# Optimization experiments

Measured on AMD Instinct MI355X. Metric: run time of the kernel, lower is better.

The kernel has to match this reference:

```python
import jax, jax.numpy as jnp
import numpy as np

NUM_TOKENS = 8192
HIDDEN = 4096
NUM_EXPERTS = 64
TOP_K = 8


def setup_inputs() -> dict:
    key = jax.random.key(0)
    k1, k2, k3 = jax.random.split(key, 3)
    tokens = jax.random.normal(k1, (NUM_TOKENS, HIDDEN), dtype=jnp.float32)
    token_probs = jax.random.uniform(k2, (NUM_TOKENS, NUM_EXPERTS), dtype=jnp.float32)
    # exactly TOP_K experts per token -> static num_out_tokens
    scores = jax.random.normal(k3, (NUM_TOKENS, NUM_EXPERTS))
    _, topk_idx = jax.lax.top_k(scores, TOP_K)  # [T, K]
    rows = jnp.arange(NUM_TOKENS)[:, None]
    routing_map = jnp.zeros((NUM_TOKENS, NUM_EXPERTS), dtype=bool).at[rows, topk_idx].set(True)
    return {
        "tokens": tokens,
        "token_probs": token_probs,
        "routing_map": routing_map,
        "num_out_tokens": NUM_TOKENS * TOP_K,
    }


def reference(tokens, token_probs, routing_map, num_out_tokens):
    # Fallback (non-fused) path of TurboTokenPermuter.forward.
    num_tokens, _ = tokens.shape
    # routing_map.bool().T -> [E, T]; masked_select in row-major order =
    # for each expert (in order), the token ids routed to it (in token order).
    flat_mask = routing_map.T.reshape(-1)  # [E*T]
    # stable argsort of ~mask puts flat positions of True entries first, in order
    perm = jnp.argsort(~flat_mask, stable=True)[:num_out_tokens]  # flat E*T indices
    sorted_indices = (perm % num_tokens).astype(jnp.int32)  # token ids (column index)
    permuted_probs = token_probs.T.reshape(-1)[perm]
    permuted_input = tokens[sorted_indices]  # index_select along dim 0
    return permuted_input, permuted_probs, sorted_indices
```

## Files before the change

### kernel.cpp

```cpp
#include <hip/hip_runtime.h>
#include <stdint.h>

#define NTOK   8192
#define NEXP   64
#define HID    4096
#define OUTROW 65536
#define CHUNK  256
#define NCHUNK (NTOK / CHUNK)
#define NPART  (NEXP * NCHUNK)

typedef float f32x4 __attribute__((ext_vector_type(4)));

__global__ void pcount_kernel(const int* __restrict__ map, int* __restrict__ pcnt) {
    int b = blockIdx.x;
    int e = b >> 5, c = b & (NCHUNK - 1);
    int lane = threadIdx.x;
    int cnt = 0;
#pragma unroll
    for (int it = 0; it < CHUNK / 64; ++it) {
        int t = c * CHUNK + it * 64 + lane;
        bool m = map[(size_t)t * NEXP + e] != 0;
        cnt += __popcll(__ballot(m));
    }
    if (lane == 0) pcnt[b] = cnt;
}

__global__ void fused_kernel(const int* __restrict__ map,
                             const float* __restrict__ probs,
                             const int* __restrict__ pcnt,
                             const float* __restrict__ tokens,
                             float* __restrict__ out_rows,
                             float* __restrict__ out_probs,
                             float* __restrict__ out_idx) {
    int b = blockIdx.x;
    int e = b >> 5, c = b & (NCHUNK - 1);
    int tid = threadIdx.x;
    int w = tid >> 6, lane = tid & 63;

    __shared__ int red[256];
    __shared__ int wcnt[4];
    __shared__ int s_src[CHUNK];

    int acc = 0;
    for (int i = tid; i < b; i += 256) acc += pcnt[i];
    red[tid] = acc;
    __syncthreads();
    for (int off = 128; off > 0; off >>= 1) {
        if (tid < off) red[tid] += red[tid + off];
        __syncthreads();
    }
    int base = red[0];

    int t = c * CHUNK + w * 64 + lane;
    bool m = map[(size_t)t * NEXP + e] != 0;
    unsigned long long bal = __ballot(m);
    int rank = __popcll(bal & ((1ull << lane) - 1ull));
    if (lane == 0) wcnt[w] = __popcll(bal);
    __syncthreads();
    int wbase = 0;
#pragma unroll
    for (int i = 0; i < 4; ++i) wbase += (i < w) ? wcnt[i] : 0;
    int total = wcnt[0] + wcnt[1] + wcnt[2] + wcnt[3];

    if (m) {
        int local = wbase + rank;
        int pos = base + local;
        out_idx[pos] = (float)t;
        out_probs[pos] = probs[(size_t)t * NEXP + e];
        s_src[local] = t;
    }
    __syncthreads();

    for (int j = w; j < total; j += 4) {
        unsigned src = (unsigned)s_src[j];
        if (src >= NTOK) src = 0;
        const f32x4* sp = (const f32x4*)(tokens + (size_t)src * HID);
        f32x4* dp = (f32x4*)(out_rows + (size_t)(base + j) * HID);
#pragma unroll
        for (int k = 0; k < HID / 4 / 64; ++k) {
            f32x4 v = sp[lane + k * 64];
            __builtin_nontemporal_store(v, dp + lane + k * 64);
        }
    }
}

extern "C" void kernel_launch(void* const* d_in, const int* in_sizes, int n_in,
                              void* d_out, int out_size, void* d_ws, size_t ws_size,
                              hipStream_t stream) {
    const float* tokens = (const float*)d_in[0];
    const float* probs  = (const float*)d_in[1];
    const int*   map    = (const int*)d_in[2];

    float* out_rows  = (float*)d_out;
    float* out_probs = out_rows + (size_t)OUTROW * HID;
    float* out_idx   = out_probs + OUTROW;

    int* pcnt = (int*)d_ws;

    pcount_kernel<<<NPART, 64, 0, stream>>>(map, pcnt);
    fused_kernel<<<NPART, CHUNK, 0, stream>>>(map, probs, pcnt, tokens,
                                              out_rows, out_probs, out_idx);
}
```

Before: 295.2 us.

## Invert gather to per-token scatter, reading each token row once

The row copy moves out of the per-expert blocks into a separate gather kernel with one block per token. An assign kernel records each token's TOPK output positions in a workspace table using atomics, and the gather kernel loads the token row once and stores it to all of its destinations. This cuts source reads from one per output row to one per token and evens out the work per block. In exchange it adds a third launch, a workspace table that must be zeroed, and atomics, and it relies on every token having exactly TOPK experts.

```diff
diff --git a/kernel.cpp b/kernel.cpp
--- a/kernel.cpp
+++ b/kernel.cpp
@@ -4,6 +4,7 @@
 #define NTOK   8192
 #define NEXP   64
 #define HID    4096
+#define TOPK   8
 #define OUTROW 65536
 #define CHUNK  256
 #define NCHUNK (NTOK / CHUNK)
@@ -11,7 +12,8 @@
 
 typedef float f32x4 __attribute__((ext_vector_type(4)));
 
-__global__ void pcount_kernel(const int* __restrict__ map, int* __restrict__ pcnt) {
+__global__ void pcount_kernel(const int* __restrict__ map, int* __restrict__ pcnt,
+                              int* __restrict__ tok_cnt) {
     int b = blockIdx.x;
     int e = b >> 5, c = b & (NCHUNK - 1);
     int lane = threadIdx.x;
@@ -19,19 +21,19 @@
 #pragma unroll
     for (int it = 0; it < CHUNK / 64; ++it) {
         int t = c * CHUNK + it * 64 + lane;
-        bool m = map[(size_t)t * NEXP + e] != 0;
-        cnt += __popcll(__ballot(m));
+        cnt += __popcll(__ballot(map[(size_t)t * NEXP + e] != 0));
     }
     if (lane == 0) pcnt[b] = cnt;
+    if (lane < NTOK / NPART) tok_cnt[b * (NTOK / NPART) + lane] = 0;
 }
 
-__global__ void fused_kernel(const int* __restrict__ map,
-                             const float* __restrict__ probs,
-                             const int* __restrict__ pcnt,
-                             const float* __restrict__ tokens,
-                             float* __restrict__ out_rows,
-                             float* __restrict__ out_probs,
-                             float* __restrict__ out_idx) {
+__global__ void assign_kernel(const int* __restrict__ map,
+                              const float* __restrict__ probs,
+                              const int* __restrict__ pcnt,
+                              int* __restrict__ tok_cnt,
+                              int* __restrict__ tok_pos,
+                              float* __restrict__ probs_out,
+                              float* __restrict__ idx_out) {
     int b = blockIdx.x;
     int e = b >> 5, c = b & (NCHUNK - 1);
     int tid = threadIdx.x;
@@ -39,7 +41,6 @@
 
     __shared__ int red[256];
     __shared__ int wcnt[4];
-    __shared__ int s_src[CHUNK];
 
     int acc = 0;
     for (int i = tid; i < b; i += 256) acc += pcnt[i];
@@ -60,27 +61,40 @@
     int wbase = 0;
 #pragma unroll
     for (int i = 0; i < 4; ++i) wbase += (i < w) ? wcnt[i] : 0;
-    int total = wcnt[0] + wcnt[1] + wcnt[2] + wcnt[3];
 
     if (m) {
-        int local = wbase + rank;
-        int pos = base + local;
-        out_idx[pos] = (float)t;
-        out_probs[pos] = probs[(size_t)t * NEXP + e];
-        s_src[local] = t;
+        int pos = base + wbase + rank;
+        idx_out[pos] = (float)t;
+        probs_out[pos] = probs[(size_t)t * NEXP + e];
+        int slot = atomicAdd(&tok_cnt[t], 1);
+        if (slot < TOPK) tok_pos[t * TOPK + slot] = pos;
     }
+}
+
+__global__ void gather_kernel(const float* __restrict__ tokens,
+                              const int* __restrict__ tok_pos,
+                              float* __restrict__ out_rows) {
+    int t = blockIdx.x;
+    int tid = threadIdx.x;
+    __shared__ int pos_s[TOPK];
+    if (tid < TOPK) pos_s[tid] = tok_pos[t * TOPK + tid];
     __syncthreads();
 
-    for (int j = w; j < total; j += 4) {
-        unsigned src = (unsigned)s_src[j];
-        if (src >= NTOK) src = 0;
-        const f32x4* sp = (const f32x4*)(tokens + (size_t)src * HID);
-        f32x4* dp = (f32x4*)(out_rows + (size_t)(base + j) * HID);
+    const f32x4* sp = (const f32x4*)(tokens + (size_t)t * HID);
+    f32x4 v0 = __builtin_nontemporal_load(sp + tid);
+    f32x4 v1 = __builtin_nontemporal_load(sp + tid + 256);
+    f32x4 v2 = __builtin_nontemporal_load(sp + tid + 512);
+    f32x4 v3 = __builtin_nontemporal_load(sp + tid + 768);
+
 #pragma unroll
-        for (int k = 0; k < HID / 4 / 64; ++k) {
-            f32x4 v = sp[lane + k * 64];
-            __builtin_nontemporal_store(v, dp + lane + k * 64);
-        }
+    for (int j = 0; j < TOPK; ++j) {
+        unsigned p = (unsigned)pos_s[j];
+        if (p >= OUTROW) continue;
+        f32x4* dp = (f32x4*)(out_rows + (size_t)p * HID);
+        __builtin_nontemporal_store(v0, dp + tid);
+        __builtin_nontemporal_store(v1, dp + tid + 256);
+        __builtin_nontemporal_store(v2, dp + tid + 512);
+        __builtin_nontemporal_store(v3, dp + tid + 768);
     }
 }
 
@@ -95,9 +109,12 @@
     float* out_probs = out_rows + (size_t)OUTROW * HID;
     float* out_idx   = out_probs + OUTROW;
 
-    int* pcnt = (int*)d_ws;
+    int* pcnt    = (int*)d_ws;
+    int* tok_cnt = pcnt + NPART;
+    int* tok_pos = tok_cnt + NTOK;
 
-    pcount_kernel<<<NPART, 64, 0, stream>>>(map, pcnt);
-    fused_kernel<<<NPART, CHUNK, 0, stream>>>(map, probs, pcnt, tokens,
-                                              out_rows, out_probs, out_idx);
+    pcount_kernel<<<NPART, 64, 0, stream>>>(map, pcnt, tok_cnt);
+    assign_kernel<<<NPART, CHUNK, 0, stream>>>(map, probs, pcnt, tok_cnt, tok_pos,
+                                               out_probs, out_idx);
+    gather_kernel<<<NTOK, 256, 0, stream>>>(tokens, tok_pos, out_rows);
 }
```

After: 268.1 us. 9.2% less time.
